# Optimization experiments

Hardware: AMD Instinct MI355X
Metric: run time of the kernel (lower is better)

The kernel has to match this reference:

```python
import jax, jax.numpy as jnp
from jax import lax
import numpy as np
import math

_DN = ('NCHW', 'OIHW', 'NCHW')
_SIGMA = 1.0
_RADIUS = int(4.0 * _SIGMA + 0.5)  # scipy truncate=4.0 default


def _gauss_kernel():
    x = jnp.arange(-_RADIUS, _RADIUS + 1, dtype=jnp.float32)
    k = jnp.exp(-0.5 * x * x / (_SIGMA * _SIGMA))
    return k / k.sum()


def _gaussian_filter(m):
    # m: [B,C,H,W]; scipy mode='reflect' == numpy pad mode 'symmetric'
    B, C, H, W = m.shape
    k = _gauss_kernel()
    x = m.reshape(B * C, 1, H, W)
    xp = jnp.pad(x, ((0, 0), (0, 0), (_RADIUS, _RADIUS), (0, 0)), mode='symmetric')
    x = lax.conv_general_dilated(xp, k.reshape(1, 1, 2 * _RADIUS + 1, 1), (1, 1), 'VALID', dimension_numbers=_DN)
    xp = jnp.pad(x, ((0, 0), (0, 0), (0, 0), (_RADIUS, _RADIUS)), mode='symmetric')
    x = lax.conv_general_dilated(xp, k.reshape(1, 1, 1, 2 * _RADIUS + 1), (1, 1), 'VALID', dimension_numbers=_DN)
    return x.reshape(B, C, H, W)


def _sobel_mag_dir(x):
    C = x.shape[1]
    sx = jnp.array([[-1, 0, 1], [-2, 0, 2], [-1, 0, 1]], dtype=jnp.float32).reshape(1, 1, 3, 3)
    sy = jnp.array([[-1, -2, -1], [0, 0, 0], [1, 2, 1]], dtype=jnp.float32).reshape(1, 1, 3, 3)
    kx = jnp.tile(sx, (C, 1, 1, 1))
    ky = jnp.tile(sy, (C, 1, 1, 1))
    gx = lax.conv_general_dilated(x, kx, (1, 1), ((1, 1), (1, 1)), dimension_numbers=_DN, feature_group_count=C)
    gy = lax.conv_general_dilated(x, ky, (1, 1), ((1, 1), (1, 1)), dimension_numbers=_DN, feature_group_count=C)
    mag = jnp.sqrt(gx * gx + gy * gy + 1e-8)
    direction = jnp.arctan2(gy, gx)
    return mag, direction


def _boundary_weight(mask_f):
    sm = jnp.clip(_gaussian_filter(mask_f), 0.0, 1.0)
    bw = 1.0 - jnp.abs(sm - 0.5) / 0.5
    return jnp.clip(bw, 0.0, 1.0)


def setup_inputs() -> dict:
    key = jax.random.key(0)
    k1, k2, k3 = jax.random.split(key, 3)
    B, C, H, W = 8, 3, 512, 512
    output = jax.random.normal(k1, (B, C, H, W), dtype=jnp.float32)
    target = jax.random.normal(k2, (B, C, H, W), dtype=jnp.float32)
    mask = jax.random.randint(k3, (B, C, H, W), 0, 2, dtype=jnp.int32)
    return {"output": output, "target": target, "mask": mask}


def reference(output, target, mask):
    mask_f = mask.astype(jnp.float32)
    out_mag, out_dir = _sobel_mag_dir(output)
    tgt_mag, tgt_dir = _sobel_mag_dir(target)
    w = _boundary_weight(mask_f)

    mag_loss = jnp.mean(jnp.abs(out_mag * w - tgt_mag * w))
    wsum = w.sum()
    mag_loss = jnp.where(wsum > 0, mag_loss / (w.mean() + 1e-8), mag_loss)

    dd = jnp.abs(out_dir - tgt_dir)
    dd = jnp.minimum(dd, 2 * math.pi - dd)
    dir_loss = (dd * w).sum()
    dir_loss = jnp.where(wsum > 0, dir_loss / (wsum + 1e-8), dir_loss)

    return mag_loss + dir_loss
```

## Files before the change

### kernel.cpp

```cpp
#include <hip/hip_runtime.h>
#include <math.h>

#define HH 512
#define WW 512
#define NBC 24
#define TH 64
#define TW 32
#define RAD 4
#define NXT (WW / TW)
#define NYT (HH / TH)
#define NBLK (NXT * NYT * NBC)
#define PI_F 3.14159265358979323846f
#define SMW 36

__device__ __constant__ float GW[9] = {
    1.3383023e-04f, 4.4318484e-03f, 5.3990968e-02f, 2.4197073e-01f,
    3.9894228e-01f, 2.4197073e-01f, 5.3990968e-02f, 4.4318484e-03f,
    1.3383023e-04f
};

__device__ __forceinline__ float abs_atan2_fast(float y, float x)
{
    float ax = fabsf(x), ay = fabsf(y);
    float mx = fmaxf(ax, ay), mn = fminf(ax, ay);
    float t = mn * __builtin_amdgcn_rcpf(fmaxf(mx, 1e-30f));
    float s = t * t;
    float r = -0.01172120f;
    r = fmaf(r, s, 0.05265332f);
    r = fmaf(r, s, -0.11643287f);
    r = fmaf(r, s, 0.19354346f);
    r = fmaf(r, s, -0.33262347f);
    r = fmaf(r, s, 0.99997726f);
    r = r * t;
    r = (ay > ax) ? (0.5f * PI_F - r) : r;
    r = (x < 0.f) ? (PI_F - r) : r;
    return r;
}

__global__ __launch_bounds__(256, 4) void egcl_fused(
    const float* __restrict__ outp,
    const float* __restrict__ tgtp,
    const int*   __restrict__ maskp,
    float*       __restrict__ partials)
{
    __shared__ __align__(16) float smh[TH + 8][SMW];
    __shared__ float red[3][4];

    const int tid = threadIdx.x;

    const int bid = (int)blockIdx.x;
    const int nb  = (bid & 7) * (NBLK / 8) + (bid >> 3);
    const int xt  = nb & 15;
    const int yt  = (nb >> 4) & 7;
    const int z   = nb >> 7;
    const int y0  = yt * TH;
    const int x0  = xt * TW;
    const size_t plane = (size_t)z * (HH * WW);
    const bool xedge = (x0 == 0) || (x0 == WW - TW);

    const int tr  = tid >> 3;
    const int c4  = (tid & 7) << 2;
    const int pr0 = tr << 1;
    const int xbase = x0 + c4;

    float Ro[4][6], Rt[4][6];
    #pragma unroll
    for (int j = 0; j < 4; ++j) {
        int gy = y0 + pr0 + j - 1;
        bool rowin = (gy >= 0) && (gy < HH);
        if (rowin) {
            const size_t rb = plane + (size_t)gy * WW;
            if (!xedge) {
                float4 vo = *(const float4*)&outp[rb + xbase];
                Ro[j][0] = outp[rb + xbase - 1];
                Ro[j][1] = vo.x; Ro[j][2] = vo.y; Ro[j][3] = vo.z; Ro[j][4] = vo.w;
                Ro[j][5] = outp[rb + xbase + 4];
                float4 vt = *(const float4*)&tgtp[rb + xbase];
                Rt[j][0] = tgtp[rb + xbase - 1];
                Rt[j][1] = vt.x; Rt[j][2] = vt.y; Rt[j][3] = vt.z; Rt[j][4] = vt.w;
                Rt[j][5] = tgtp[rb + xbase + 4];
            } else {
                #pragma unroll
                for (int k = 0; k < 6; ++k) {
                    int gx = xbase - 1 + k;
                    bool in = (gx >= 0) && (gx < WW);
                    size_t idx = rb + (in ? gx : 0);
                    Ro[j][k] = in ? outp[idx] : 0.f;
                    Rt[j][k] = in ? tgtp[idx] : 0.f;
                }
            }
        } else {
            #pragma unroll
            for (int k = 0; k < 6; ++k) { Ro[j][k] = 0.f; Rt[j][k] = 0.f; }
        }
    }

    for (int i = tid; i < (TH + 8) * 8; i += 256) {
        int r = i >> 3, cg = (i & 7) << 2;
        int gy = y0 + r - RAD;
        gy = (gy < 0) ? (-gy - 1) : ((gy >= HH) ? (2 * HH - 1 - gy) : gy);
        const int* mrow = maskp + plane + (size_t)gy * WW;
        float win[12];
        if (!xedge) {
            int4 a = *(const int4*)&mrow[x0 + cg - 4];
            int4 b = *(const int4*)&mrow[x0 + cg];
            int4 c = *(const int4*)&mrow[x0 + cg + 4];
            win[0] = (float)a.x; win[1]  = (float)a.y; win[2]  = (float)a.z; win[3]  = (float)a.w;
            win[4] = (float)b.x; win[5]  = (float)b.y; win[6]  = (float)b.z; win[7]  = (float)b.w;
            win[8] = (float)c.x; win[9]  = (float)c.y; win[10] = (float)c.z; win[11] = (float)c.w;
        } else {
            #pragma unroll
            for (int k = 0; k < 12; ++k) {
                int gx = x0 + cg - 4 + k;
                gx = (gx < 0) ? (-gx - 1) : ((gx >= WW) ? (2 * WW - 1 - gx) : gx);
                win[k] = (float)mrow[gx];
            }
        }
        float s0 = 0.f, s1 = 0.f, s2 = 0.f, s3 = 0.f;
        #pragma unroll
        for (int j = 0; j < 9; ++j) {
            float gw = GW[j];
            s0 = fmaf(gw, win[j],     s0);
            s1 = fmaf(gw, win[j + 1], s1);
            s2 = fmaf(gw, win[j + 2], s2);
            s3 = fmaf(gw, win[j + 3], s3);
        }
        *(float4*)&smh[r][cg] = make_float4(s0, s1, s2, s3);
    }
    __syncthreads();

    float4 a0 = make_float4(0.f, 0.f, 0.f, 0.f);
    float4 a1 = a0;
    #pragma unroll
    for (int j = 0; j < 10; ++j) {
        float4 m = *(const float4*)&smh[pr0 + j][c4];
        if (j < 9) {
            float gw = GW[j];
            a0.x = fmaf(gw, m.x, a0.x); a0.y = fmaf(gw, m.y, a0.y);
            a0.z = fmaf(gw, m.z, a0.z); a0.w = fmaf(gw, m.w, a0.w);
        }
        if (j > 0) {
            float gw = GW[j - 1];
            a1.x = fmaf(gw, m.x, a1.x); a1.y = fmaf(gw, m.y, a1.y);
            a1.z = fmaf(gw, m.z, a1.z); a1.w = fmaf(gw, m.w, a1.w);
        }
    }
    float wgt[2][4];
    {
        float smv[2][4] = {{a0.x, a0.y, a0.z, a0.w}, {a1.x, a1.y, a1.z, a1.w}};
        #pragma unroll
        for (int p = 0; p < 2; ++p)
            #pragma unroll
            for (int i = 0; i < 4; ++i) {
                float sm = fminf(fmaxf(smv[p][i], 0.f), 1.f);
                float w = 1.f - fabsf(sm - 0.5f) * 2.f;
                wgt[p][i] = fminf(fmaxf(w, 0.f), 1.f);
            }
    }

    float gxo[2][4], gyo[2][4], gxt[2][4], gyt[2][4];
    {
        float t0[6], t1[6], u0[6], u1[6];
        #pragma unroll
        for (int j = 0; j < 6; ++j) {
            t0[j] = fmaf(2.f, Ro[1][j], Ro[0][j] + Ro[2][j]);
            t1[j] = fmaf(2.f, Ro[2][j], Ro[1][j] + Ro[3][j]);
            u0[j] = Ro[2][j] - Ro[0][j];
            u1[j] = Ro[3][j] - Ro[1][j];
        }
        #pragma unroll
        for (int i = 0; i < 4; ++i) {
            gxo[0][i] = t0[i + 2] - t0[i];
            gxo[1][i] = t1[i + 2] - t1[i];
            gyo[0][i] = fmaf(2.f, u0[i + 1], u0[i] + u0[i + 2]);
            gyo[1][i] = fmaf(2.f, u1[i + 1], u1[i] + u1[i + 2]);
        }
        #pragma unroll
        for (int j = 0; j < 6; ++j) {
            t0[j] = fmaf(2.f, Rt[1][j], Rt[0][j] + Rt[2][j]);
            t1[j] = fmaf(2.f, Rt[2][j], Rt[1][j] + Rt[3][j]);
            u0[j] = Rt[2][j] - Rt[0][j];
            u1[j] = Rt[3][j] - Rt[1][j];
        }
        #pragma unroll
        for (int i = 0; i < 4; ++i) {
            gxt[0][i] = t0[i + 2] - t0[i];
            gxt[1][i] = t1[i + 2] - t1[i];
            gyt[0][i] = fmaf(2.f, u0[i + 1], u0[i] + u0[i + 2]);
            gyt[1][i] = fmaf(2.f, u1[i + 1], u1[i] + u1[i + 2]);
        }
    }

    float s_w = 0.f, s_mag = 0.f, s_dir = 0.f;
    #pragma unroll
    for (int p = 0; p < 2; ++p) {
        #pragma unroll
        for (int i = 0; i < 4; ++i) {
            float xo = gxo[p][i], yo = gyo[p][i];
            float xt_ = gxt[p][i], yt_ = gyt[p][i];
            float mago = __builtin_amdgcn_sqrtf(fmaf(xo, xo, fmaf(yo, yo, 1e-8f)));
            float magt = __builtin_amdgcn_sqrtf(fmaf(xt_, xt_, fmaf(yt_, yt_, 1e-8f)));
            float cross = yo * xt_ - xo * yt_;
            float dotp  = fmaf(xo, xt_, yo * yt_);
            float dd = abs_atan2_fast(cross, dotp);
            float w = wgt[p][i];
            s_w   += w;
            s_mag += w * fabsf(mago - magt);
            s_dir += dd * w;
        }
    }

    #pragma unroll
    for (int o = 32; o > 0; o >>= 1) {
        s_w   += __shfl_down(s_w,   o, 64);
        s_mag += __shfl_down(s_mag, o, 64);
        s_dir += __shfl_down(s_dir, o, 64);
    }
    const int wid = tid >> 6;
    if ((tid & 63) == 0) { red[0][wid] = s_w; red[1][wid] = s_mag; red[2][wid] = s_dir; }
    __syncthreads();
    if (tid == 0) {
        partials[bid]            = red[0][0] + red[0][1] + red[0][2] + red[0][3];
        partials[NBLK + bid]     = red[1][0] + red[1][1] + red[1][2] + red[1][3];
        partials[2 * NBLK + bid] = red[2][0] + red[2][1] + red[2][2] + red[2][3];
    }
}

__global__ __launch_bounds__(256) void egcl_finalize(
    const float* __restrict__ partials, float* __restrict__ out)
{
    __shared__ double red[3][4];
    const int tid = threadIdx.x;
    double s0 = 0.0, s1 = 0.0, s2 = 0.0;
    const float4* p0 = (const float4*)partials;
    const float4* p1 = (const float4*)(partials + NBLK);
    const float4* p2 = (const float4*)(partials + 2 * NBLK);
    for (int i = tid; i < NBLK / 4; i += 256) {
        float4 a = p0[i], b = p1[i], c = p2[i];
        s0 += (double)a.x + (double)a.y + (double)a.z + (double)a.w;
        s1 += (double)b.x + (double)b.y + (double)b.z + (double)b.w;
        s2 += (double)c.x + (double)c.y + (double)c.z + (double)c.w;
    }
    #pragma unroll
    for (int o = 32; o > 0; o >>= 1) {
        s0 += __shfl_down(s0, o, 64);
        s1 += __shfl_down(s1, o, 64);
        s2 += __shfl_down(s2, o, 64);
    }
    const int wid = tid >> 6;
    if ((tid & 63) == 0) { red[0][wid] = s0; red[1][wid] = s1; red[2][wid] = s2; }
    __syncthreads();
    if (tid == 0) {
        double Sw   = red[0][0] + red[0][1] + red[0][2] + red[0][3];
        double Smag = red[1][0] + red[1][1] + red[1][2] + red[1][3];
        double Sdir = red[2][0] + red[2][1] + red[2][2] + red[2][3];
        const double N = (double)NBC * HH * WW;
        double mag_loss = Smag / N;
        if (Sw > 0.0) mag_loss = mag_loss / (Sw / N + 1e-8);
        double dir_loss = Sdir;
        if (Sw > 0.0) dir_loss = Sdir / (Sw + 1e-8);
        out[0] = (float)(mag_loss + dir_loss);
    }
}

extern "C" void kernel_launch(void* const* d_in, const int* in_sizes, int n_in,
                              void* d_out, int out_size, void* d_ws, size_t ws_size,
                              hipStream_t stream)
{
    const float* outp = (const float*)d_in[0];
    const float* tgtp = (const float*)d_in[1];
    const int*   maskp = (const int*)d_in[2];
    float* partials = (float*)d_ws;

    egcl_fused<<<dim3(NBLK, 1, 1), 256, 0, stream>>>(outp, tgtp, maskp, partials);
    egcl_finalize<<<1, 256, 0, stream>>>(partials, (float*)d_out);
}
```

Before: 38.83 us.

## Make each wave own its own mask-blur tile and drop block barriers

Each 64-lane wave now computes its own 24-row horizontally blurred mask strip in a private shared-memory slice. This replaces the block-wide cooperative strip and its __syncthreads with a wave-local lgkmcnt wait. Per-wave partial sums go straight to global memory, which removes the second block barrier, and the finalize kernel grows to 1024 threads to reduce the four-times-larger partial array. The cost is redundant halo work, since each wave blurs 24 rows for 16 outputs instead of sharing 72 rows across 64. Correctness also relies on wave-level lockstep ordering of the LDS writes and reads.

```diff
diff --git a/kernel.cpp b/kernel.cpp
--- a/kernel.cpp
+++ b/kernel.cpp
@@ -10,6 +10,7 @@
 #define NXT (WW / TW)
 #define NYT (HH / TH)
 #define NBLK (NXT * NYT * NBC)
+#define NWAVE (NBLK * 4)
 #define PI_F 3.14159265358979323846f
 #define SMW 36
 
@@ -43,30 +44,32 @@
     const int*   __restrict__ maskp,
     float*       __restrict__ partials)
 {
-    __shared__ __align__(16) float smh[TH + 8][SMW];
-    __shared__ float red[3][4];
-
-    const int tid = threadIdx.x;
+    __shared__ __align__(16) float smh[4][24][SMW];
+
+    const int tid  = threadIdx.x;
+    const int lane = tid & 63;
+    const int wv   = tid >> 6;
 
     const int bid = (int)blockIdx.x;
     const int nb  = (bid & 7) * (NBLK / 8) + (bid >> 3);
     const int xt  = nb & 15;
     const int yt  = (nb >> 4) & 7;
     const int z   = nb >> 7;
-    const int y0  = yt * TH;
     const int x0  = xt * TW;
+    const int wy0 = yt * TH + wv * 16;
     const size_t plane = (size_t)z * (HH * WW);
     const bool xedge = (x0 == 0) || (x0 == WW - TW);
 
-    const int tr  = tid >> 3;
-    const int c4  = (tid & 7) << 2;
-    const int pr0 = tr << 1;
+    const int cg  = lane & 7;
+    const int c4  = cg << 2;
+    const int rp  = lane >> 3;
+    const int pr0 = rp << 1;
     const int xbase = x0 + c4;
 
     float Ro[4][6], Rt[4][6];
     #pragma unroll
     for (int j = 0; j < 4; ++j) {
-        int gy = y0 + pr0 + j - 1;
+        int gy = wy0 + pr0 + j - 1;
         bool rowin = (gy >= 0) && (gy < HH);
         if (rowin) {
             const size_t rb = plane + (size_t)gy * WW;
@@ -95,23 +98,25 @@
         }
     }
 
-    for (int i = tid; i < (TH + 8) * 8; i += 256) {
-        int r = i >> 3, cg = (i & 7) << 2;
-        int gy = y0 + r - RAD;
+    #pragma unroll
+    for (int it = 0; it < 3; ++it) {
+        int i = lane + (it << 6);
+        int r = i >> 3, cgs = (i & 7) << 2;
+        int gy = wy0 + r - RAD;
         gy = (gy < 0) ? (-gy - 1) : ((gy >= HH) ? (2 * HH - 1 - gy) : gy);
         const int* mrow = maskp + plane + (size_t)gy * WW;
         float win[12];
         if (!xedge) {
-            int4 a = *(const int4*)&mrow[x0 + cg - 4];
-            int4 b = *(const int4*)&mrow[x0 + cg];
-            int4 c = *(const int4*)&mrow[x0 + cg + 4];
+            int4 a = *(const int4*)&mrow[x0 + cgs - 4];
+            int4 b = *(const int4*)&mrow[x0 + cgs];
+            int4 c = *(const int4*)&mrow[x0 + cgs + 4];
             win[0] = (float)a.x; win[1]  = (float)a.y; win[2]  = (float)a.z; win[3]  = (float)a.w;
             win[4] = (float)b.x; win[5]  = (float)b.y; win[6]  = (float)b.z; win[7]  = (float)b.w;
             win[8] = (float)c.x; win[9]  = (float)c.y; win[10] = (float)c.z; win[11] = (float)c.w;
         } else {
             #pragma unroll
             for (int k = 0; k < 12; ++k) {
-                int gx = x0 + cg - 4 + k;
+                int gx = x0 + cgs - 4 + k;
                 gx = (gx < 0) ? (-gx - 1) : ((gx >= WW) ? (2 * WW - 1 - gx) : gx);
                 win[k] = (float)mrow[gx];
             }
@@ -125,15 +130,16 @@
             s2 = fmaf(gw, win[j + 2], s2);
             s3 = fmaf(gw, win[j + 3], s3);
         }
-        *(float4*)&smh[r][cg] = make_float4(s0, s1, s2, s3);
-    }
-    __syncthreads();
+        *(float4*)&smh[wv][r][cgs] = make_float4(s0, s1, s2, s3);
+    }
+
+    asm volatile("s_waitcnt lgkmcnt(0)" ::: "memory");
 
     float4 a0 = make_float4(0.f, 0.f, 0.f, 0.f);
     float4 a1 = a0;
     #pragma unroll
     for (int j = 0; j < 10; ++j) {
-        float4 m = *(const float4*)&smh[pr0 + j][c4];
+        float4 m = *(const float4*)&smh[wv][pr0 + j][c4];
         if (j < 9) {
             float gw = GW[j];
             a0.x = fmaf(gw, m.x, a0.x); a0.y = fmaf(gw, m.y, a0.y);
@@ -216,26 +222,24 @@
         s_mag += __shfl_down(s_mag, o, 64);
         s_dir += __shfl_down(s_dir, o, 64);
     }
-    const int wid = tid >> 6;
-    if ((tid & 63) == 0) { red[0][wid] = s_w; red[1][wid] = s_mag; red[2][wid] = s_dir; }
-    __syncthreads();
-    if (tid == 0) {
-        partials[bid]            = red[0][0] + red[0][1] + red[0][2] + red[0][3];
-        partials[NBLK + bid]     = red[1][0] + red[1][1] + red[1][2] + red[1][3];
-        partials[2 * NBLK + bid] = red[2][0] + red[2][1] + red[2][2] + red[2][3];
-    }
-}
-
-__global__ __launch_bounds__(256) void egcl_finalize(
+    if (lane == 0) {
+        const int wix = (bid << 2) | wv;
+        partials[wix]             = s_w;
+        partials[NWAVE + wix]     = s_mag;
+        partials[2 * NWAVE + wix] = s_dir;
+    }
+}
+
+__global__ __launch_bounds__(1024) void egcl_finalize(
     const float* __restrict__ partials, float* __restrict__ out)
 {
-    __shared__ double red[3][4];
+    __shared__ double red[3][16];
     const int tid = threadIdx.x;
     double s0 = 0.0, s1 = 0.0, s2 = 0.0;
     const float4* p0 = (const float4*)partials;
-    const float4* p1 = (const float4*)(partials + NBLK);
-    const float4* p2 = (const float4*)(partials + 2 * NBLK);
-    for (int i = tid; i < NBLK / 4; i += 256) {
+    const float4* p1 = (const float4*)(partials + NWAVE);
+    const float4* p2 = (const float4*)(partials + 2 * NWAVE);
+    for (int i = tid; i < NWAVE / 4; i += 1024) {
         float4 a = p0[i], b = p1[i], c = p2[i];
         s0 += (double)a.x + (double)a.y + (double)a.z + (double)a.w;
         s1 += (double)b.x + (double)b.y + (double)b.z + (double)b.w;
@@ -251,9 +255,9 @@
     if ((tid & 63) == 0) { red[0][wid] = s0; red[1][wid] = s1; red[2][wid] = s2; }
     __syncthreads();
     if (tid == 0) {
-        double Sw   = red[0][0] + red[0][1] + red[0][2] + red[0][3];
-        double Smag = red[1][0] + red[1][1] + red[1][2] + red[1][3];
-        double Sdir = red[2][0] + red[2][1] + red[2][2] + red[2][3];
+        double Sw = 0.0, Smag = 0.0, Sdir = 0.0;
+        #pragma unroll
+        for (int k = 0; k < 16; ++k) { Sw += red[0][k]; Smag += red[1][k]; Sdir += red[2][k]; }
         const double N = (double)NBC * HH * WW;
         double mag_loss = Smag / N;
         if (Sw > 0.0) mag_loss = mag_loss / (Sw / N + 1e-8);
@@ -273,5 +277,5 @@
     float* partials = (float*)d_ws;
 
     egcl_fused<<<dim3(NBLK, 1, 1), 256, 0, stream>>>(outp, tgtp, maskp, partials);
-    egcl_finalize<<<1, 256, 0, stream>>>(partials, (float*)d_out);
-}
+    egcl_finalize<<<1, 1024, 0, stream>>>(partials, (float*)d_out);
+}
```

New measurement: 39.87 us. +2.7%, slower.
